# Optimization experiments

Hardware: AMD Instinct MI355X
Metric: run time of the kernel (lower is better)

Reference implementation:

```python
import jax, jax.numpy as jnp
import numpy as np

N_NODES = 50000
N_EDGES = 640000
N_GRAPHS = 64
D_IN = 3
D_H = 128
N_CLASSES = 10
EPS = 1e-5


def setup_inputs() -> dict:
    key = jax.random.key(0)
    ks = jax.random.split(key, 32)
    inp = {
        "x": jax.random.normal(ks[0], (N_NODES, D_IN), dtype=jnp.float32),
        "src": jax.random.randint(ks[1], (N_EDGES,), 0, N_NODES, dtype=jnp.int32),
        "dst": jax.random.randint(ks[2], (N_EDGES,), 0, N_NODES, dtype=jnp.int32),
        "batch": jnp.sort(jax.random.randint(ks[3], (N_NODES,), 0, N_GRAPHS, dtype=jnp.int32)),
        "enc_w": jax.random.normal(ks[4], (D_IN, D_H), dtype=jnp.float32) * 0.1,
        "enc_b": jnp.zeros((D_H,), jnp.float32),
        "fc_w": jax.random.normal(ks[5], (D_H, D_H), dtype=jnp.float32) * 0.05,
        "fc_b": jnp.zeros((D_H,), jnp.float32),
        "pred_w": jax.random.normal(ks[6], (D_H, N_CLASSES), dtype=jnp.float32) * 0.05,
        "pred_b": jnp.zeros((N_CLASSES,), jnp.float32),
    }
    for i in range(4):
        inp[f"w{i}"] = jax.random.normal(ks[8 + i], (D_H, D_H), dtype=jnp.float32) * 0.05
        inp[f"b{i}"] = jnp.zeros((D_H,), jnp.float32)
        inp[f"ln_w{i}"] = jnp.ones((D_H,), jnp.float32)
        inp[f"ln_b{i}"] = jnp.zeros((D_H,), jnp.float32)
    return inp


def _gcn_norm(src, dst, n):
    # add self-loops, symmetric deg^{-1/2} normalization (GCNConv default)
    loop = jnp.arange(n, dtype=src.dtype)
    src_f = jnp.concatenate([src, loop])
    dst_f = jnp.concatenate([dst, loop])
    deg = jax.ops.segment_sum(jnp.ones_like(dst_f, jnp.float32), dst_f, num_segments=n)
    dinv = jnp.where(deg > 0, 1.0 / jnp.sqrt(deg), 0.0)
    norm = dinv[src_f] * dinv[dst_f]
    return src_f, dst_f, norm


def _gcn(x, w, b, src_f, dst_f, norm, n):
    h = x @ w                           # [N, D]
    m = h[src_f] * norm[:, None]        # gather + scale  [E+N, D]
    return jax.ops.segment_sum(m, dst_f, num_segments=n) + b


def _graph_ln(x, w, b):
    # PyG LayerNorm mode='graph', batch=None: normalize over ALL nodes+channels
    mu = x.mean()
    sd = jnp.sqrt(((x - mu) ** 2).mean())
    return (x - mu) / (sd + EPS) * w + b


def reference(x, src, dst, batch, enc_w, enc_b, fc_w, fc_b, pred_w, pred_b,
              w0, b0, ln_w0, ln_b0, w1, b1, ln_w1, ln_b1,
              w2, b2, ln_w2, ln_b2, w3, b3, ln_w3, ln_b3):
    n = x.shape[0]
    src_f, dst_f, norm = _gcn_norm(src, dst, n)
    h = jax.nn.elu(x @ enc_w + enc_b)   # input encoder (Linear + ELU)
    convs = [(w0, b0, ln_w0, ln_b0), (w1, b1, ln_w1, ln_b1),
             (w2, b2, ln_w2, ln_b2), (w3, b3, ln_w3, ln_b3)]
    for w, b, lw, lb in convs:
        h = _gcn(h, w, b, src_f, dst_f, norm, n)
        h = jax.nn.relu(h)
        h = _graph_ln(h, lw, lb)
    g = jax.ops.segment_max(h, batch, num_segments=N_GRAPHS)  # global_max_pool
    g = jnp.tanh(g @ fc_w + fc_b)
    return g @ pred_w + pred_b
```

## Files before the change

### kernel.cpp

```cpp
#include <hip/hip_runtime.h>
#include <cfloat>
#include <cmath>

#define D 128
#define D4 32
#define LB 32

typedef __attribute__((ext_vector_type(8))) short short8;
typedef __attribute__((ext_vector_type(4))) float f32x4;

__device__ __forceinline__ float4 f4fma(float s, float4 a, float4 acc) {
    acc.x = fmaf(s, a.x, acc.x);
    acc.y = fmaf(s, a.y, acc.y);
    acc.z = fmaf(s, a.z, acc.z);
    acc.w = fmaf(s, a.w, acc.w);
    return acc;
}

__device__ __forceinline__ unsigned short f2bf(float x) {
    unsigned int b = __float_as_uint(x);
    unsigned int r = (b + 0x7FFFu + ((b >> 16) & 1u)) >> 16;
    return (unsigned short)r;
}

__device__ __forceinline__ unsigned int pack2bf(float a, float b) {
    return (unsigned int)f2bf(a) | ((unsigned int)f2bf(b) << 16);
}

__device__ __forceinline__ float bf2f(unsigned short u) {
    return __uint_as_float(((unsigned int)u) << 16);
}

__device__ __forceinline__ void accum8(float* a, float nrm, uint4 t) {
    a[0] = fmaf(nrm, bf2f((unsigned short)(t.x & 0xFFFFu)), a[0]);
    a[1] = fmaf(nrm, bf2f((unsigned short)(t.x >> 16)), a[1]);
    a[2] = fmaf(nrm, bf2f((unsigned short)(t.y & 0xFFFFu)), a[2]);
    a[3] = fmaf(nrm, bf2f((unsigned short)(t.y >> 16)), a[3]);
    a[4] = fmaf(nrm, bf2f((unsigned short)(t.z & 0xFFFFu)), a[4]);
    a[5] = fmaf(nrm, bf2f((unsigned short)(t.z >> 16)), a[5]);
    a[6] = fmaf(nrm, bf2f((unsigned short)(t.w & 0xFFFFu)), a[6]);
    a[7] = fmaf(nrm, bf2f((unsigned short)(t.w >> 16)), a[7]);
}

__global__ void k_pre(const float* __restrict__ x, const float* __restrict__ ew,
                      const float* __restrict__ eb, unsigned short* __restrict__ h,
                      const int* __restrict__ dst, int* __restrict__ cnt,
                      const float* __restrict__ w0, const float* __restrict__ w1,
                      const float* __restrict__ w2, const float* __restrict__ w3,
                      unsigned short* __restrict__ wt,
                      int N, int E, int EB, int CB) {
    int b = blockIdx.x;
    if (b < EB) {
        int idx = b * 256 + threadIdx.x;
        if (idx >= N * D4) return;
        int n = idx >> 5, c4 = idx & 31;
        const float4* w4 = (const float4*)ew;
        float4 b4 = ((const float4*)eb)[c4];
        float x0 = x[n * 3 + 0], x1 = x[n * 3 + 1], x2 = x[n * 3 + 2];
        float4 v = b4;
        v = f4fma(x0, w4[0 * D4 + c4], v);
        v = f4fma(x1, w4[1 * D4 + c4], v);
        v = f4fma(x2, w4[2 * D4 + c4], v);
        v.x = v.x > 0.f ? v.x : expm1f(v.x);
        v.y = v.y > 0.f ? v.y : expm1f(v.y);
        v.z = v.z > 0.f ? v.z : expm1f(v.z);
        v.w = v.w > 0.f ? v.w : expm1f(v.w);
        ushort4 o;
        o.x = f2bf(v.x); o.y = f2bf(v.y); o.z = f2bf(v.z); o.w = f2bf(v.w);
        ((ushort4*)h)[idx] = o;
    } else if (b < EB + CB) {
        int i = (b - EB) * 256 + threadIdx.x;
        if (i < E) atomicAdd(&cnt[dst[i]], 1);
    } else {
        int bb = b - EB - CB;
        int l = bb >> 3, blk = bb & 7;
        const float* w = (l == 0) ? w0 : (l == 1) ? w1 : (l == 2) ? w2 : w3;
        unsigned short* wtl = wt + (size_t)l * D * D;
        int nl = threadIdx.x & 15;
        int ck = threadIdx.x >> 4;
        int n = blk * 16 + nl;
        unsigned int p[4];
        #pragma unroll
        for (int q = 0; q < 4; ++q) {
            int k0 = ck * 8 + 2 * q;
            p[q] = pack2bf(w[(k0 + 0) * D + n], w[(k0 + 1) * D + n]);
        }
        ((uint4*)(wtl + (size_t)n * D))[ck] = make_uint4(p[0], p[1], p[2], p[3]);
    }
}

__global__ void k_scanall(const int* __restrict__ cnt, int* __restrict__ rowptr,
                          int* __restrict__ cur, float* __restrict__ dinv,
                          int N, int NB) {
    __shared__ int pre[256];
    int b = blockIdx.x, t = threadIdx.x;
    int limit = b * 256;
    int s = 0;
    for (int i = t; i < limit; i += 256) s += cnt[i];
    pre[t] = s;
    __syncthreads();
    for (int off = 128; off; off >>= 1) {
        if (t < off) pre[t] += pre[t + off];
        __syncthreads();
    }
    int base = pre[0];
    __syncthreads();
    int i = b * 256 + t;
    int v = (i < N) ? cnt[i] : 0;
    pre[t] = v;
    __syncthreads();
    for (int off = 1; off < 256; off <<= 1) {
        int u = (t >= off) ? pre[t - off] : 0;
        __syncthreads();
        pre[t] += u;
        __syncthreads();
    }
    if (i < N) {
        int excl = base + ((t == 0) ? 0 : pre[t - 1]);
        rowptr[i] = excl;
        cur[i] = excl;
        dinv[i] = 1.0f / sqrtf((float)v + 1.0f);
    }
    if (b == NB - 1 && t == 255) rowptr[N] = base + pre[255];
}

__global__ void k_fill(const int* __restrict__ src, const int* __restrict__ dst,
                       const float* __restrict__ dinv, int* __restrict__ cur,
                       int2* __restrict__ edata, int E) {
    int e = blockIdx.x * blockDim.x + threadIdx.x;
    if (e >= E) return;
    int s = src[e], d = dst[e];
    int p = atomicAdd(&cur[d], 1);
    edata[p] = make_int2(s, __float_as_int(dinv[s] * dinv[d]));
}

__launch_bounds__(256)
__global__ void k_layer(const unsigned short* __restrict__ Ain,
                        const unsigned short* __restrict__ wt,
                        const float* __restrict__ lwp, const float* __restrict__ lbp,
                        const double* __restrict__ sums_prev,
                        const float* __restrict__ bias,
                        const int2* __restrict__ edata, const int* __restrict__ rowptr,
                        const float* __restrict__ dinv,
                        unsigned short* __restrict__ Aout,
                        double* __restrict__ sums, int N) {
    __shared__ uint4 a_lds4[512];
    __shared__ float s_sh[D], o_sh[D];
    __shared__ float ss[4], sq[4];
    char* a_lds = (char*)a_lds4;
    int row0 = blockIdx.x * LB;

    if (threadIdx.x < D) {
        float s = 1.f, o = 0.f;
        if (lwp) {
            double M = (double)N * D;
            double m = sums_prev[0] / M;
            double var = sums_prev[1] / M - m * m;
            float sd = sqrtf(var > 0.0 ? (float)var : 0.f);
            float inv = 1.f / (sd + 1e-5f);
            s = inv * lwp[threadIdx.x];
            o = lbp[threadIdx.x] - (float)m * s;
        }
        s_sh[threadIdx.x] = s;
        o_sh[threadIdx.x] = o;
    }
    __syncthreads();

    int g = threadIdx.x >> 4;
    int lane = threadIdx.x & 15;
    const uint4* T16 = (const uint4*)Ain;
    for (int k = 0; k < 2; ++k) {
        int nl = g * 2 + k;
        int n = row0 + nl;
        if (n < N) {
            int e0 = rowptr[n], e1 = rowptr[n + 1];
            float acc[8];
            #pragma unroll
            for (int q = 0; q < 8; ++q) acc[q] = 0.f;
            float rsum = 0.f;
            int e = e0;
            for (; e + 8 <= e1; e += 8) {
                int2 ed[8]; uint4 tv[8];
                #pragma unroll
                for (int j = 0; j < 8; ++j) ed[j] = edata[e + j];
                #pragma unroll
                for (int j = 0; j < 8; ++j) tv[j] = T16[(size_t)ed[j].x * 16 + lane];
                #pragma unroll
                for (int j = 0; j < 8; ++j) {
                    float nm = __int_as_float(ed[j].y);
                    accum8(acc, nm, tv[j]);
                    rsum += nm;
                }
            }
            for (; e + 4 <= e1; e += 4) {
                int2 ed[4]; uint4 tv[4];
                #pragma unroll
                for (int j = 0; j < 4; ++j) ed[j] = edata[e + j];
                #pragma unroll
                for (int j = 0; j < 4; ++j) tv[j] = T16[(size_t)ed[j].x * 16 + lane];
                #pragma unroll
                for (int j = 0; j < 4; ++j) {
                    float nm = __int_as_float(ed[j].y);
                    accum8(acc, nm, tv[j]);
                    rsum += nm;
                }
            }
            for (; e < e1; ++e) {
                int2 d = edata[e];
                float nm = __int_as_float(d.y);
                accum8(acc, nm, T16[(size_t)d.x * 16 + lane]);
                rsum += nm;
            }
            float di = dinv[n];
            float sl = di * di;
            accum8(acc, sl, T16[(size_t)n * 16 + lane]);
            rsum += sl;
            float v[8];
            #pragma unroll
            for (int q = 0; q < 8; ++q) {
                int ch = 8 * lane + q;
                v[q] = fmaf(s_sh[ch], acc[q], rsum * o_sh[ch]);
            }
            int i = nl * 16 + lane;
            int byte = (i << 4) ^ ((nl & 7) << 4);
            *(uint4*)(a_lds + byte) = make_uint4(pack2bf(v[0], v[1]),
                                                 pack2bf(v[2], v[3]),
                                                 pack2bf(v[4], v[5]),
                                                 pack2bf(v[6], v[7]));
        }
    }
    __syncthreads();

    int wv = threadIdx.x >> 6;
    int l64 = threadIdx.x & 63;
    int lrow = l64 & 15;
    int kg = l64 >> 4;
    int rt = wv & 1;
    int cb = wv >> 1;

    f32x4 acc2[4];
    #pragma unroll
    for (int ct = 0; ct < 4; ++ct) acc2[ct] = (f32x4){0.f, 0.f, 0.f, 0.f};

    #pragma unroll
    for (int ks = 0; ks < 4; ++ks) {
        int ar = rt * 16 + lrow;
        int abyte = (ar * 256 + ks * 64 + kg * 16) ^ ((ar & 7) << 4);
        short8 a = *(short8*)(a_lds + abyte);
        #pragma unroll
        for (int ct = 0; ct < 4; ++ct) {
            int col = cb * 64 + ct * 16 + lrow;
            short8 b = *(const short8*)(wt + (size_t)col * D + ks * 32 + kg * 8);
            acc2[ct] = __builtin_amdgcn_mfma_f32_16x16x32_bf16(a, b, acc2[ct], 0, 0, 0);
        }
    }

    float ls = 0.f, lq = 0.f;
    #pragma unroll
    for (int ct = 0; ct < 4; ++ct) {
        int col = cb * 64 + ct * 16 + lrow;
        float bb = bias[col];
        #pragma unroll
        for (int r = 0; r < 4; ++r) {
            int rtile = rt * 16 + kg * 4 + r;
            int row = row0 + rtile;
            if (row < N) {
                float v = acc2[ct][r] + bb;
                v = fmaxf(v, 0.f);
                Aout[(size_t)row * D + col] = f2bf(v);
                ls += v;
                lq += v * v;
            }
        }
    }
    for (int off = 32; off; off >>= 1) {
        ls += __shfl_down(ls, off);
        lq += __shfl_down(lq, off);
    }
    if (l64 == 0) { ss[wv] = ls; sq[wv] = lq; }
    __syncthreads();
    if (threadIdx.x == 0) {
        float S = ss[0] + ss[1] + ss[2] + ss[3];
        float Q = sq[0] + sq[1] + sq[2] + sq[3];
        atomicAdd(&sums[0], (double)S);
        atomicAdd(&sums[1], (double)Q);
    }
}

__launch_bounds__(512)
__global__ void k_tail(const unsigned short* __restrict__ A, const int* __restrict__ batch,
                       const float* __restrict__ lw, const float* __restrict__ lb,
                       const double* __restrict__ sums,
                       const float* __restrict__ fc_w, const float* __restrict__ fc_b,
                       const float* __restrict__ pred_w, const float* __restrict__ pred_b,
                       float* __restrict__ out, int N) {
    int gi = blockIdx.x;
    int lo = 0, hi = N;
    while (lo < hi) { int mid = (lo + hi) >> 1; if (batch[mid] < gi) lo = mid + 1; else hi = mid; }
    int start = lo;
    hi = N;
    while (lo < hi) { int mid = (lo + hi) >> 1; if (batch[mid] < gi + 1) lo = mid + 1; else hi = mid; }
    int end = lo;

    int c = threadIdx.x & 127, sub = threadIdx.x >> 7;
    double M = (double)N * D;
    double m_ = sums[0] / M;
    double var = sums[1] / M - m_ * m_;
    float sd = sqrtf(var > 0.0 ? (float)var : 0.f);
    float inv = 1.f / (sd + 1e-5f);
    float s = inv * lw[c];
    float o = lb[c] - (float)m_ * s;

    float mx = -FLT_MAX;
    for (int node = start + sub; node < end; node += 4)
        mx = fmaxf(mx, fmaf(bf2f(A[(size_t)node * D + c]), s, o));

    __shared__ float red[4][128];
    __shared__ float gm[128], tr[128];
    red[sub][c] = mx;
    __syncthreads();
    if (sub == 0)
        gm[c] = fmaxf(fmaxf(red[0][c], red[1][c]), fmaxf(red[2][c], red[3][c]));
    __syncthreads();
    if (threadIdx.x < 128) {
        float acc = fc_b[c];
        for (int k = 0; k < D; ++k) acc = fmaf(gm[k], fc_w[k * D + c], acc);
        tr[c] = tanhf(acc);
    }
    __syncthreads();
    if (threadIdx.x < 10) {
        int j = threadIdx.x;
        float acc = pred_b[j];
        for (int k = 0; k < D; ++k) acc = fmaf(tr[k], pred_w[k * 10 + j], acc);
        out[gi * 10 + j] = acc;
    }
}

extern "C" void kernel_launch(void* const* d_in, const int* in_sizes, int n_in,
                              void* d_out, int out_size, void* d_ws, size_t ws_size,
                              hipStream_t stream) {
    const float* x      = (const float*)d_in[0];
    const int*   src    = (const int*)d_in[1];
    const int*   dst    = (const int*)d_in[2];
    const int*   batch  = (const int*)d_in[3];
    const float* enc_w  = (const float*)d_in[4];
    const float* enc_b  = (const float*)d_in[5];
    const float* fc_w   = (const float*)d_in[6];
    const float* fc_b   = (const float*)d_in[7];
    const float* pred_w = (const float*)d_in[8];
    const float* pred_b = (const float*)d_in[9];

    int N = in_sizes[0] / 3;
    int E = in_sizes[1];
    int G = out_size / 10;
    int NB = (N + 255) / 256;

    char* ws = (char*)d_ws;
    size_t off = 0;
    auto align512 = [](size_t v) { return (v + 511) / 512 * 512; };
    int*   cnt    = (int*)(ws + off);   off += align512((size_t)N * 4);
    double* sums  = (double*)(ws + off); off += 512;
    float* dinv   = (float*)(ws + off); off += align512((size_t)N * 4);
    int*   rowptr = (int*)(ws + off);   off += align512(((size_t)N + 1) * 4);
    int*   cur    = (int*)(ws + off);   off += align512((size_t)N * 4);
    int2*  edata  = (int2*)(ws + off);  off += align512((size_t)E * 8);
    unsigned short* A0 = (unsigned short*)(ws + off); off += align512((size_t)N * D * 2);
    unsigned short* A1 = (unsigned short*)(ws + off); off += align512((size_t)N * D * 2);
    unsigned short* wt = (unsigned short*)(ws + off); off += align512((size_t)4 * D * D * 2);

    const float* wL[4], *bL[4], *lwL[4], *lbL[4];
    for (int L = 0; L < 4; ++L) {
        wL[L]  = (const float*)d_in[10 + 4 * L];
        bL[L]  = (const float*)d_in[11 + 4 * L];
        lwL[L] = (const float*)d_in[12 + 4 * L];
        lbL[L] = (const float*)d_in[13 + 4 * L];
    }

    hipMemsetAsync(cnt, 0, align512((size_t)N * 4) + 512, stream);
    int EB = (N * D4 + 255) / 256;
    int CB = (E + 255) / 256;
    k_pre<<<EB + CB + 32, 256, 0, stream>>>(x, enc_w, enc_b, A0, dst, cnt,
                                            wL[0], wL[1], wL[2], wL[3], wt,
                                            N, E, EB, CB);
    k_scanall<<<NB, 256, 0, stream>>>(cnt, rowptr, cur, dinv, N, NB);
    k_fill<<<(E + 255) / 256, 256, 0, stream>>>(src, dst, dinv, cur, edata, E);

    int NBL = (N + LB - 1) / LB;
    unsigned short* Ain = A0;
    unsigned short* Aout = A1;
    for (int L = 0; L < 4; ++L) {
        const float* lwp = L ? lwL[L - 1] : nullptr;
        const float* lbp = L ? lbL[L - 1] : nullptr;
        k_layer<<<NBL, 256, 0, stream>>>(Ain, wt + (size_t)L * D * D,
                                         lwp, lbp, &sums[2 * (L ? L - 1 : 0)],
                                         bL[L], edata, rowptr, dinv,
                                         Aout, &sums[2 * L], N);
        unsigned short* tmp = Ain; Ain = Aout; Aout = tmp;
    }

    k_tail<<<G, 512, 0, stream>>>(Ain, batch, lwL[3], lbL[3], &sums[6],
                                  fc_w, fc_b, pred_w, pred_b, (float*)d_out, N);
}
```

Before: 529.1 us.

## Halve layer row tile to 16 and split graph max-pool across blocks

Each layer block now covers 16 rows instead of 32. Every 16-thread group aggregates one node, and each wave computes a 16x32 MFMA output slice. This doubles the block count to raise occupancy and parallelism in the gather-bound aggregation. The tail is split into a pooling kernel that uses 8 blocks per graph to write partial maxima and a small kernel that reduces them and applies the MLP, which adds a launch and a workspace buffer. Global atomic sum traffic per layer also doubles.

```diff
diff --git a/kernel.cpp b/kernel.cpp
--- a/kernel.cpp
+++ b/kernel.cpp
@@ -4,7 +4,7 @@
 
 #define D 128
 #define D4 32
-#define LB 32
+#define LB 16
 
 typedef __attribute__((ext_vector_type(8))) short short8;
 typedef __attribute__((ext_vector_type(4))) float f32x4;
@@ -144,7 +144,7 @@
                         const float* __restrict__ dinv,
                         unsigned short* __restrict__ Aout,
                         double* __restrict__ sums, int N) {
-    __shared__ uint4 a_lds4[512];
+    __shared__ uint4 a_lds4[256];
     __shared__ float s_sh[D], o_sh[D];
     __shared__ float ss[4], sq[4];
     char* a_lds = (char*)a_lds4;
@@ -166,68 +166,65 @@
     }
     __syncthreads();
 
-    int g = threadIdx.x >> 4;
+    int nl = threadIdx.x >> 4;
     int lane = threadIdx.x & 15;
     const uint4* T16 = (const uint4*)Ain;
-    for (int k = 0; k < 2; ++k) {
-        int nl = g * 2 + k;
-        int n = row0 + nl;
-        if (n < N) {
-            int e0 = rowptr[n], e1 = rowptr[n + 1];
-            float acc[8];
-            #pragma unroll
-            for (int q = 0; q < 8; ++q) acc[q] = 0.f;
-            float rsum = 0.f;
-            int e = e0;
-            for (; e + 8 <= e1; e += 8) {
-                int2 ed[8]; uint4 tv[8];
-                #pragma unroll
-                for (int j = 0; j < 8; ++j) ed[j] = edata[e + j];
-                #pragma unroll
-                for (int j = 0; j < 8; ++j) tv[j] = T16[(size_t)ed[j].x * 16 + lane];
-                #pragma unroll
-                for (int j = 0; j < 8; ++j) {
-                    float nm = __int_as_float(ed[j].y);
-                    accum8(acc, nm, tv[j]);
-                    rsum += nm;
-                }
-            }
-            for (; e + 4 <= e1; e += 4) {
-                int2 ed[4]; uint4 tv[4];
-                #pragma unroll
-                for (int j = 0; j < 4; ++j) ed[j] = edata[e + j];
-                #pragma unroll
-                for (int j = 0; j < 4; ++j) tv[j] = T16[(size_t)ed[j].x * 16 + lane];
-                #pragma unroll
-                for (int j = 0; j < 4; ++j) {
-                    float nm = __int_as_float(ed[j].y);
-                    accum8(acc, nm, tv[j]);
-                    rsum += nm;
-                }
-            }
-            for (; e < e1; ++e) {
-                int2 d = edata[e];
-                float nm = __int_as_float(d.y);
-                accum8(acc, nm, T16[(size_t)d.x * 16 + lane]);
+    int n = row0 + nl;
+    if (n < N) {
+        int e0 = rowptr[n], e1 = rowptr[n + 1];
+        float acc[8];
+        #pragma unroll
+        for (int q = 0; q < 8; ++q) acc[q] = 0.f;
+        float rsum = 0.f;
+        int e = e0;
+        for (; e + 8 <= e1; e += 8) {
+            int2 ed[8]; uint4 tv[8];
+            #pragma unroll
+            for (int j = 0; j < 8; ++j) ed[j] = edata[e + j];
+            #pragma unroll
+            for (int j = 0; j < 8; ++j) tv[j] = T16[(size_t)ed[j].x * 16 + lane];
+            #pragma unroll
+            for (int j = 0; j < 8; ++j) {
+                float nm = __int_as_float(ed[j].y);
+                accum8(acc, nm, tv[j]);
                 rsum += nm;
             }
-            float di = dinv[n];
-            float sl = di * di;
-            accum8(acc, sl, T16[(size_t)n * 16 + lane]);
-            rsum += sl;
-            float v[8];
-            #pragma unroll
-            for (int q = 0; q < 8; ++q) {
-                int ch = 8 * lane + q;
-                v[q] = fmaf(s_sh[ch], acc[q], rsum * o_sh[ch]);
+        }
+        for (; e + 4 <= e1; e += 4) {
+            int2 ed[4]; uint4 tv[4];
+            #pragma unroll
+            for (int j = 0; j < 4; ++j) ed[j] = edata[e + j];
+            #pragma unroll
+            for (int j = 0; j < 4; ++j) tv[j] = T16[(size_t)ed[j].x * 16 + lane];
+            #pragma unroll
+            for (int j = 0; j < 4; ++j) {
+                float nm = __int_as_float(ed[j].y);
+                accum8(acc, nm, tv[j]);
+                rsum += nm;
             }
-            int i = nl * 16 + lane;
-            int byte = (i << 4) ^ ((nl & 7) << 4);
-            *(uint4*)(a_lds + byte) = make_uint4(pack2bf(v[0], v[1]),
-                                                 pack2bf(v[2], v[3]),
-                                                 pack2bf(v[4], v[5]),
-                                                 pack2bf(v[6], v[7]));
-        }
+        }
+        for (; e < e1; ++e) {
+            int2 d = edata[e];
+            float nm = __int_as_float(d.y);
+            accum8(acc, nm, T16[(size_t)d.x * 16 + lane]);
+            rsum += nm;
+        }
+        float di = dinv[n];
+        float sl = di * di;
+        accum8(acc, sl, T16[(size_t)n * 16 + lane]);
+        rsum += sl;
+        float v[8];
+        #pragma unroll
+        for (int q = 0; q < 8; ++q) {
+            int ch = 8 * lane + q;
+            v[q] = fmaf(s_sh[ch], acc[q], rsum * o_sh[ch]);
+        }
+        int i = nl * 16 + lane;
+        int byte = (i << 4) ^ ((nl & 7) << 4);
+        *(uint4*)(a_lds + byte) = make_uint4(pack2bf(v[0], v[1]),
+                                             pack2bf(v[2], v[3]),
+                                             pack2bf(v[4], v[5]),
+                                             pack2bf(v[6], v[7]));
     }
     __syncthreads();
 
@@ -235,21 +232,18 @@
     int l64 = threadIdx.x & 63;
     int lrow = l64 & 15;
     int kg = l64 >> 4;
-    int rt = wv & 1;
-    int cb = wv >> 1;
-
-    f32x4 acc2[4];
+
+    f32x4 acc2[2];
     #pragma unroll
-    for (int ct = 0; ct < 4; ++ct) acc2[ct] = (f32x4){0.f, 0.f, 0.f, 0.f};
+    for (int ct = 0; ct < 2; ++ct) acc2[ct] = (f32x4){0.f, 0.f, 0.f, 0.f};
 
     #pragma unroll
     for (int ks = 0; ks < 4; ++ks) {
-        int ar = rt * 16 + lrow;
-        int abyte = (ar * 256 + ks * 64 + kg * 16) ^ ((ar & 7) << 4);
+        int abyte = (lrow * 256 + ks * 64 + kg * 16) ^ ((lrow & 7) << 4);
         short8 a = *(short8*)(a_lds + abyte);
         #pragma unroll
-        for (int ct = 0; ct < 4; ++ct) {
-            int col = cb * 64 + ct * 16 + lrow;
+        for (int ct = 0; ct < 2; ++ct) {
+            int col = wv * 32 + ct * 16 + lrow;
             short8 b = *(const short8*)(wt + (size_t)col * D + ks * 32 + kg * 8);
             acc2[ct] = __builtin_amdgcn_mfma_f32_16x16x32_bf16(a, b, acc2[ct], 0, 0, 0);
         }
@@ -257,12 +251,12 @@
 
     float ls = 0.f, lq = 0.f;
     #pragma unroll
-    for (int ct = 0; ct < 4; ++ct) {
-        int col = cb * 64 + ct * 16 + lrow;
+    for (int ct = 0; ct < 2; ++ct) {
+        int col = wv * 32 + ct * 16 + lrow;
         float bb = bias[col];
         #pragma unroll
         for (int r = 0; r < 4; ++r) {
-            int rtile = rt * 16 + kg * 4 + r;
+            int rtile = kg * 4 + r;
             int row = row0 + rtile;
             if (row < N) {
                 float v = acc2[ct][r] + bb;
@@ -287,14 +281,11 @@
     }
 }
 
-__launch_bounds__(512)
-__global__ void k_tail(const unsigned short* __restrict__ A, const int* __restrict__ batch,
+__launch_bounds__(256)
+__global__ void k_pool(const unsigned short* __restrict__ A, const int* __restrict__ batch,
                        const float* __restrict__ lw, const float* __restrict__ lb,
-                       const double* __restrict__ sums,
-                       const float* __restrict__ fc_w, const float* __restrict__ fc_b,
-                       const float* __restrict__ pred_w, const float* __restrict__ pred_b,
-                       float* __restrict__ out, int N) {
-    int gi = blockIdx.x;
+                       const double* __restrict__ sums, float* __restrict__ pmax, int N) {
+    int gi = blockIdx.x >> 3, part = blockIdx.x & 7;
     int lo = 0, hi = N;
     while (lo < hi) { int mid = (lo + hi) >> 1; if (batch[mid] < gi) lo = mid + 1; else hi = mid; }
     int start = lo;
@@ -312,27 +303,37 @@
     float o = lb[c] - (float)m_ * s;
 
     float mx = -FLT_MAX;
-    for (int node = start + sub; node < end; node += 4)
+    for (int node = start + part * 2 + sub; node < end; node += 16)
         mx = fmaxf(mx, fmaf(bf2f(A[(size_t)node * D + c]), s, o));
 
-    __shared__ float red[4][128];
+    __shared__ float red[2][128];
+    red[sub][c] = mx;
+    __syncthreads();
+    if (sub == 0)
+        pmax[(size_t)blockIdx.x * D + c] = fmaxf(red[0][c], red[1][c]);
+}
+
+__launch_bounds__(128)
+__global__ void k_tail2(const float* __restrict__ pmax,
+                        const float* __restrict__ fc_w, const float* __restrict__ fc_b,
+                        const float* __restrict__ pred_w, const float* __restrict__ pred_b,
+                        float* __restrict__ out) {
+    int gi = blockIdx.x, c = threadIdx.x;
     __shared__ float gm[128], tr[128];
-    red[sub][c] = mx;
-    __syncthreads();
-    if (sub == 0)
-        gm[c] = fmaxf(fmaxf(red[0][c], red[1][c]), fmaxf(red[2][c], red[3][c]));
-    __syncthreads();
-    if (threadIdx.x < 128) {
-        float acc = fc_b[c];
-        for (int k = 0; k < D; ++k) acc = fmaf(gm[k], fc_w[k * D + c], acc);
-        tr[c] = tanhf(acc);
-    }
-    __syncthreads();
-    if (threadIdx.x < 10) {
-        int j = threadIdx.x;
-        float acc = pred_b[j];
-        for (int k = 0; k < D; ++k) acc = fmaf(tr[k], pred_w[k * 10 + j], acc);
-        out[gi * 10 + j] = acc;
+    float mx = -FLT_MAX;
+    #pragma unroll
+    for (int p = 0; p < 8; ++p)
+        mx = fmaxf(mx, pmax[(size_t)(gi * 8 + p) * D + c]);
+    gm[c] = mx;
+    __syncthreads();
+    float acc = fc_b[c];
+    for (int k = 0; k < D; ++k) acc = fmaf(gm[k], fc_w[k * D + c], acc);
+    tr[c] = tanhf(acc);
+    __syncthreads();
+    if (c < 10) {
+        float a2 = pred_b[c];
+        for (int k = 0; k < D; ++k) a2 = fmaf(tr[k], pred_w[k * 10 + c], a2);
+        out[gi * 10 + c] = a2;
     }
 }
 
@@ -367,6 +368,7 @@
     unsigned short* A0 = (unsigned short*)(ws + off); off += align512((size_t)N * D * 2);
     unsigned short* A1 = (unsigned short*)(ws + off); off += align512((size_t)N * D * 2);
     unsigned short* wt = (unsigned short*)(ws + off); off += align512((size_t)4 * D * D * 2);
+    float* pmax   = (float*)(ws + off); off += align512((size_t)G * 8 * D * 4);
 
     const float* wL[4], *bL[4], *lwL[4], *lbL[4];
     for (int L = 0; L < 4; ++L) {
@@ -398,6 +400,6 @@
         unsigned short* tmp = Ain; Ain = Aout; Aout = tmp;
     }
 
-    k_tail<<<G, 512, 0, stream>>>(Ain, batch, lwL[3], lbL[3], &sums[6],
-                                  fc_w, fc_b, pred_w, pred_b, (float*)d_out, N);
-}
+    k_pool<<<G * 8, 256, 0, stream>>>(Ain, batch, lwL[3], lbL[3], &sums[6], pmax, N);
+    k_tail2<<<G, 128, 0, stream>>>(pmax, fc_w, fc_b, pred_w, pred_b, (float*)d_out);
+}
```

New measurement: 613.2 us. 15.9% more time.
